# Kernel optimization log

Measured on AMD Instinct MI355X. Metric: run time of the kernel, lower is better.

Reference implementation:

```python
import jax, jax.numpy as jnp
import numpy as np

NUM_HEADS = 16
NUM_KV_HEADS = 4
HEAD_DIM = 128
BASE_THETA = 10000.0


def _rope_cos_sin(seq_len, head_dim, dtype):
    # standard (ntk_alpha=1) rotate-half RoPE tables: [S, head_dim]
    inv_freq = 1.0 / (BASE_THETA ** (jnp.arange(0, head_dim, 2, dtype=jnp.float32) / head_dim))
    angles = jnp.arange(seq_len, dtype=jnp.float32)[:, None] * inv_freq[None, :]  # [S, D/2]
    cos = jnp.concatenate([jnp.cos(angles), jnp.cos(angles)], axis=-1).astype(dtype)
    sin = jnp.concatenate([jnp.sin(angles), jnp.sin(angles)], axis=-1).astype(dtype)
    return cos, sin


def _rotate_half(t):
    half = t.shape[-1] // 2
    return jnp.concatenate([-t[..., half:], t[..., :half]], axis=-1)


def setup_inputs() -> dict:
    key = jax.random.key(0)
    ks = jax.random.split(key, 5)
    B, S, E = 2, 2048, 2048
    KV = NUM_KV_HEADS * HEAD_DIM  # 512
    scale = 0.02
    return {
        "x": jax.random.normal(ks[0], (B, S, E), dtype=jnp.float32),
        "Wq": jax.random.normal(ks[1], (E, E), dtype=jnp.float32) * scale,
        "Wk": jax.random.normal(ks[2], (E, KV), dtype=jnp.float32) * scale,
        "Wv": jax.random.normal(ks[3], (E, KV), dtype=jnp.float32) * scale,
        "Wo": jax.random.normal(ks[4], (E, E), dtype=jnp.float32) * scale,
    }


def reference(x, Wq, Wk, Wv, Wo):
    B, S, E = x.shape
    n_rep = NUM_HEADS // NUM_KV_HEADS
    scale = 1.0 / jnp.sqrt(jnp.float32(HEAD_DIM))

    # QKV projections (bias=False)
    q = (x @ Wq).reshape(B, S, NUM_HEADS, HEAD_DIM)
    k = (x @ Wk).reshape(B, S, NUM_KV_HEADS, HEAD_DIM)
    v = (x @ Wv).reshape(B, S, NUM_KV_HEADS, HEAD_DIM)

    # dynamic RoPE on q, k
    cos, sin = _rope_cos_sin(S, HEAD_DIM, x.dtype)
    cos = cos[None, :, None, :]
    sin = sin[None, :, None, :]
    q = q * cos + _rotate_half(q) * sin
    k = k * cos + _rotate_half(k) * sin

    # GQA: repeat kv heads to match query heads
    k = jnp.repeat(k, n_rep, axis=2)
    v = jnp.repeat(v, n_rep, axis=2)

    # [B, H, S, D]
    q = q.transpose(0, 2, 1, 3)
    k = k.transpose(0, 2, 1, 3)
    v = v.transpose(0, 2, 1, 3)

    # causal mask (window_size=0 -> standard causal, additive float mask)
    i = jnp.arange(S)[:, None]
    j = jnp.arange(S)[None, :]
    neg = jnp.finfo(jnp.float32).min
    causal = jnp.where(j > i, neg, 0.0).astype(jnp.float32)  # [S, S]

    scores = jnp.einsum("bhqd,bhkd->bhqk", q, k) * scale
    scores = scores + causal[None, None, :, :]
    weights = jax.nn.softmax(scores.astype(jnp.float32), axis=-1)
    attn = jnp.einsum("bhqk,bhkd->bhqd", weights.astype(v.dtype), v)

    attn = attn.transpose(0, 2, 1, 3).reshape(B, S, E)
    return attn @ Wo
```

## Files before the change

### kernel.cpp

```cpp
#include <hip/hip_runtime.h>
#include <math.h>


typedef __attribute__((ext_vector_type(8))) short short8;
typedef __attribute__((ext_vector_type(4))) float f32x4;

typedef const __attribute__((address_space(1))) void* gvp;
typedef __attribute__((address_space(3))) void* svp;

__device__ __forceinline__ void async16(const void* g, void* l) {
  __builtin_amdgcn_global_load_lds((gvp)g, (svp)l, 16, 0, 0);
}
__device__ __forceinline__ void wait_vm0() { asm volatile("s_waitcnt vmcnt(0)" ::: "memory"); }
__device__ __forceinline__ void barrier_raw() { asm volatile("s_barrier" ::: "memory"); }

__device__ __forceinline__ unsigned short f2b(float f) {
  unsigned int u = __builtin_bit_cast(unsigned int, f);
  u += 0x7fffu + ((u >> 16) & 1u);
  return (unsigned short)(u >> 16);
}
__device__ __forceinline__ float b2f(unsigned short h) {
  unsigned int u = ((unsigned int)h) << 16;
  return __builtin_bit_cast(float, u);
}

__global__ __launch_bounds__(256) void convx(const float* __restrict__ x,
                                             unsigned short* __restrict__ xb) {
  int i = blockIdx.x * 256 + threadIdx.x;
  const float4* p = (const float4*)x + (size_t)i * 2;
  float4 a = p[0], b4 = p[1];
  union { short8 v; unsigned short u[8]; } o;
  o.u[0] = f2b(a.x);  o.u[1] = f2b(a.y);  o.u[2] = f2b(a.z);  o.u[3] = f2b(a.w);
  o.u[4] = f2b(b4.x); o.u[5] = f2b(b4.y); o.u[6] = f2b(b4.z); o.u[7] = f2b(b4.w);
  ((short8*)xb)[i] = o.v;
}

__global__ __launch_bounds__(256) void wconv_all(const float* __restrict__ Wq,
                                                 const float* __restrict__ Wk,
                                                 const float* __restrict__ Wv,
                                                 const float* __restrict__ Wo,
                                                 unsigned short* __restrict__ WqkvT,
                                                 unsigned short* __restrict__ WoT) {
  __shared__ float t[32][33];
  int idx = blockIdx.x;
  const float* W; unsigned short* WT; int N, tx, ty;
  const int K = 2048;
  if (idx < 4096)      { W = Wq; WT = WqkvT;                         N = 2048; idx -= 0;    tx = idx & 63; ty = idx >> 6; }
  else if (idx < 5120) { W = Wk; WT = WqkvT + (size_t)2048 * 2048;   N = 512;  idx -= 4096; tx = idx & 15; ty = idx >> 4; }
  else if (idx < 6144) { W = Wv; WT = WqkvT + (size_t)2560 * 2048;   N = 512;  idx -= 5120; tx = idx & 15; ty = idx >> 4; }
  else                 { W = Wo; WT = WoT;                           N = 2048; idx -= 6144; tx = idx & 63; ty = idx >> 6; }
  int c = threadIdx.x & 31, r0 = threadIdx.x >> 5;
  int k0 = ty * 32, n0 = tx * 32;
#pragma unroll
  for (int r = r0; r < 32; r += 8) t[r][c] = W[(size_t)(k0 + r) * N + n0 + c];
  __syncthreads();
#pragma unroll
  for (int r = r0; r < 32; r += 8) WT[(size_t)(n0 + r) * K + k0 + c] = f2b(t[c][r]);
}

__global__ __launch_bounds__(256) void gemm_bt(const unsigned short* __restrict__ A,
                                               const unsigned short* __restrict__ BT,
                                               void* __restrict__ Cout,
                                               int M, int N, int K, int out_bf16) {
  const int n0 = blockIdx.x * 128;
  const int m0 = blockIdx.y * 128;
  const int tid = threadIdx.x;
  const int w = tid >> 6, lane = tid & 63, l15 = lane & 15, quad = lane >> 4;
  const int wm = w >> 1, wn = w & 1;

  __shared__ __align__(16) unsigned short As[2][128 * 64];
  __shared__ __align__(16) unsigned short Bs[2][128 * 64];

  f32x4 acc[4][4];
#pragma unroll
  for (int mi = 0; mi < 4; mi++)
#pragma unroll
    for (int ni = 0; ni < 4; ni++) acc[mi][ni] = (f32x4){0.f, 0.f, 0.f, 0.f};

  const int rl = lane >> 3;
  const int cl = lane & 7;
  const unsigned short* Ab = A + (size_t)m0 * K;
  const unsigned short* Bb = BT + (size_t)n0 * K;

#pragma unroll
  for (int i = 0; i < 4; i++) {
    int row = w * 32 + i * 8 + rl;
    int gc = cl ^ (row & 7);
    async16(Ab + (size_t)row * K + gc * 8, &As[0][(w * 32 + i * 8) * 64]);
    async16(Bb + (size_t)row * K + gc * 8, &Bs[0][(w * 32 + i * 8) * 64]);
  }

  const int nIter = K >> 6;
  for (int j = 0; j < nIter; j++) {
    wait_vm0();
    barrier_raw();
    const int cur = j & 1;

    if (j + 1 < nIter) {
      int kb = (j + 1) * 64;
#pragma unroll
      for (int i = 0; i < 4; i++) {
        int row = w * 32 + i * 8 + rl;
        int gc = cl ^ (row & 7);
        async16(Ab + (size_t)row * K + kb + gc * 8, &As[cur ^ 1][(w * 32 + i * 8) * 64]);
        async16(Bb + (size_t)row * K + kb + gc * 8, &Bs[cur ^ 1][(w * 32 + i * 8) * 64]);
      }
    }

    const unsigned short* as = &As[cur][0];
    const unsigned short* bs = &Bs[cur][0];
#pragma unroll
    for (int kk = 0; kk < 2; kk++) {
      short8 af[4], bfv[4];
#pragma unroll
      for (int mi = 0; mi < 4; mi++) {
        int row = wm * 64 + mi * 16 + l15;
        af[mi] = *(const short8*)&as[row * 64 + (((kk * 4 + quad) ^ (row & 7)) * 8)];
      }
#pragma unroll
      for (int ni = 0; ni < 4; ni++) {
        int row = wn * 64 + ni * 16 + l15;
        bfv[ni] = *(const short8*)&bs[row * 64 + (((kk * 4 + quad) ^ (row & 7)) * 8)];
      }
#pragma unroll
      for (int mi = 0; mi < 4; mi++)
#pragma unroll
        for (int ni = 0; ni < 4; ni++)
          acc[mi][ni] = __builtin_amdgcn_mfma_f32_16x16x32_bf16(af[mi], bfv[ni],
                                                                acc[mi][ni], 0, 0, 0);
    }
  }

  if (out_bf16) {
    unsigned short* C = (unsigned short*)Cout;
#pragma unroll
    for (int mi = 0; mi < 4; mi++)
#pragma unroll
      for (int ni = 0; ni < 4; ni++)
#pragma unroll
        for (int r = 0; r < 4; r++) {
          int row = m0 + wm * 64 + mi * 16 + quad * 4 + r;
          int col = n0 + wn * 64 + ni * 16 + l15;
          C[(size_t)row * N + col] = f2b(acc[mi][ni][r]);
        }
  } else {
    float* C = (float*)Cout;
#pragma unroll
    for (int mi = 0; mi < 4; mi++)
#pragma unroll
      for (int ni = 0; ni < 4; ni++)
#pragma unroll
        for (int r = 0; r < 4; r++) {
          int row = m0 + wm * 64 + mi * 16 + quad * 4 + r;
          int col = n0 + wn * 64 + ni * 16 + l15;
          C[(size_t)row * N + col] = acc[mi][ni][r];
        }
  }
}

#define SC_TOT 0.12753785056274918f
__global__ __launch_bounds__(256) void rope_kernel(const unsigned short* __restrict__ qkv,
                                                   unsigned short* __restrict__ Q,
                                                   unsigned short* __restrict__ Kd) {
  int b = blockIdx.z, hh = blockIdx.y;
  int tid = threadIdx.x;
  int d = tid & 63, sl = tid >> 6;
  int s = blockIdx.x * 4 + sl;
  const unsigned short* src = qkv + ((size_t)(b * 2048 + s)) * 3072 + hh * 128;
  float lo = b2f(src[d]), hi = b2f(src[d + 64]);
  float invf = exp2f(-0.20762050593046f * (float)d);
  float ang = (float)s * invf;
  float sn, cs;
  sincosf(ang, &sn, &cs);
  float nlo = lo * cs - hi * sn;
  float nhi = hi * cs + lo * sn;
  unsigned short* dst;
  if (hh < 16) {
    nlo *= SC_TOT; nhi *= SC_TOT;
    dst = Q + ((size_t)((b * 16 + hh) * 2048 + s)) * 128;
  } else {
    dst = Kd + ((size_t)((b * 4 + (hh - 16)) * 2048 + s)) * 128;
  }
  dst[d] = f2b(nlo);
  dst[d + 64] = f2b(nhi);
}

__global__ __launch_bounds__(256) void vtrans(const unsigned short* __restrict__ qkv,
                                              unsigned short* __restrict__ Vt) {
  int bkv = blockIdx.z;
  int b = bkv >> 2, kv = bkv & 3;
  int s0 = blockIdx.x * 64, d0 = blockIdx.y * 64;
  __shared__ unsigned short t[64][65];
  int c = threadIdx.x & 63, r0 = threadIdx.x >> 6;
  const unsigned short* src = qkv + ((size_t)(b * 2048 + s0)) * 3072 + 2560 + kv * 128 + d0;
#pragma unroll
  for (int r = r0; r < 64; r += 4) t[r][c] = src[(size_t)r * 3072 + c];
  __syncthreads();
  unsigned short* dst = Vt + ((size_t)bkv * 128 + d0) * 2048 + s0;
#pragma unroll
  for (int r = r0; r < 64; r += 4) dst[(size_t)r * 2048 + c] = t[c][r];
}

#define FIXED_M 12.0f
__global__ __launch_bounds__(256) void flash2(const unsigned short* __restrict__ Q,
                                              const unsigned short* __restrict__ Kc,
                                              const unsigned short* __restrict__ Vt,
                                              unsigned short* __restrict__ attn) {
  const int pair = blockIdx.x;
  const int h = blockIdx.y;
  const int b = blockIdx.z;
  const int kvh = h >> 2;
  const int tid = threadIdx.x;
  const int w = tid >> 6, lane = tid & 63, l15 = lane & 15, quad = lane >> 4;

  __shared__ __align__(16) unsigned short kbuf[2][64 * 128];
  __shared__ __align__(16) unsigned short vbuf[2][128 * 64];
  __shared__ __align__(16) unsigned short pbuf[4][16 * 64];

  const unsigned short* Qb = Q  + ((size_t)(b * 16 + h)) * 2048 * 128;
  const unsigned short* Kb = Kc + ((size_t)(b * 4 + kvh)) * 2048 * 128;
  const unsigned short* Vb = Vt + ((size_t)(b * 4 + kvh)) * 128 * 2048;
  unsigned short* pb = &pbuf[w][0];

  for (int t = 0; t < 2; t++) {
    const int qt = (t == 0) ? pair : (31 - pair);
    const int q0 = qt * 64;
    const int nT = qt + 1;

    short8 qf[4];
    {
      const unsigned short* qp = Qb + (size_t)(q0 + w * 16 + l15) * 128 + quad * 8;
#pragma unroll
      for (int kk = 0; kk < 4; kk++) qf[kk] = *(const short8*)(qp + kk * 32);
    }

    float l_i[4];
    f32x4 o[8];
#pragma unroll
    for (int r = 0; r < 4; r++) l_i[r] = 0.f;
#pragma unroll
    for (int nn = 0; nn < 8; nn++) o[nn] = (f32x4){0.f, 0.f, 0.f, 0.f};

    barrier_raw();

#pragma unroll
    for (int k = 0; k < 4; k++) {
      int m = w * 4 + k;
      int rl = m * 4 + (lane >> 4);
      int c8 = (lane & 15) ^ (rl & 7);
      async16(Kb + (size_t)rl * 128 + c8 * 8, &kbuf[0][m * 512]);
    }
#pragma unroll
    for (int k = 0; k < 4; k++) {
      int m = w * 4 + k;
      int d = m * 8 + (lane >> 3);
      int c3 = (lane & 7) ^ (d & 7);
      async16(Vb + (size_t)d * 2048 + c3 * 8, &vbuf[0][m * 512]);
    }

    for (int j = 0; j < nT; j++) {
      wait_vm0();
      barrier_raw();
      const int cur = j & 1;

      if (j + 1 < nT) {
        int j1 = (j + 1) * 64;
#pragma unroll
        for (int k = 0; k < 4; k++) {
          int m = w * 4 + k;
          int rl = m * 4 + (lane >> 4);
          int c8 = (lane & 15) ^ (rl & 7);
          async16(Kb + (size_t)(j1 + rl) * 128 + c8 * 8, &kbuf[cur ^ 1][m * 512]);
        }
#pragma unroll
        for (int k = 0; k < 4; k++) {
          int m = w * 4 + k;
          int d = m * 8 + (lane >> 3);
          int c3 = (lane & 7) ^ (d & 7);
          async16(Vb + (size_t)d * 2048 + (j + 1) * 64 + c3 * 8, &vbuf[cur ^ 1][m * 512]);
        }
      }

      const unsigned short* kb = &kbuf[cur][0];
      const unsigned short* vb = &vbuf[cur][0];

      f32x4 s4[4];
#pragma unroll
      for (int nn = 0; nn < 4; nn++) {
        f32x4 a = (f32x4){0.f, 0.f, 0.f, 0.f};
        int row = nn * 16 + l15;
#pragma unroll
        for (int kk = 0; kk < 4; kk++) {
          short8 bfr = *(const short8*)&kb[row * 128 + (((kk * 4 + quad) ^ (row & 7)) * 8)];
          a = __builtin_amdgcn_mfma_f32_16x16x32_bf16(qf[kk], bfr, a, 0, 0, 0);
        }
        s4[nn] = a;
      }

      const bool diag = (j * 64 == q0);
      const int myrow = w * 16 + quad * 4;
#pragma unroll
      for (int nn = 0; nn < 4; nn++) {
        int col = nn * 16 + l15;
#pragma unroll
        for (int r = 0; r < 4; r++) {
          float p = exp2f(s4[nn][r] - FIXED_M);
          if (diag && (col > myrow + r)) p = 0.f;
          l_i[r] += p;
          int prow = quad * 4 + r;
          pb[prow * 64 + ((nn * 2 + (l15 >> 3)) ^ (prow & 7)) * 8 + (l15 & 7)] = f2b(p);
        }
      }

#pragma unroll
      for (int ks = 0; ks < 2; ks++) {
        short8 af = *(const short8*)&pb[l15 * 64 + (((ks * 4 + quad) ^ (l15 & 7)) * 8)];
#pragma unroll
        for (int nn = 0; nn < 8; nn++) {
          int d = nn * 16 + l15;
          short8 bfr = *(const short8*)&vb[d * 64 + (((ks * 4 + quad) ^ (d & 7)) * 8)];
          o[nn] = __builtin_amdgcn_mfma_f32_16x16x32_bf16(af, bfr, o[nn], 0, 0, 0);
        }
      }
    }

#pragma unroll
    for (int r = 0; r < 4; r++) {
#pragma unroll
      for (int off = 1; off < 16; off <<= 1) l_i[r] += __shfl_xor(l_i[r], off, 64);
    }
    float inv[4];
#pragma unroll
    for (int r = 0; r < 4; r++) inv[r] = 1.f / l_i[r];
    unsigned short* ap = attn + ((size_t)(b * 2048 + q0 + w * 16)) * 2048 + h * 128;
#pragma unroll
    for (int nn = 0; nn < 8; nn++)
#pragma unroll
      for (int r = 0; r < 4; r++)
        ap[(size_t)(quad * 4 + r) * 2048 + nn * 16 + l15] = f2b(o[nn][r] * inv[r]);
  }
}

extern "C" void kernel_launch(void* const* d_in, const int* in_sizes, int n_in,
                              void* d_out, int out_size, void* d_ws, size_t ws_size,
                              hipStream_t stream) {
  const float* x  = (const float*)d_in[0];
  const float* Wq = (const float*)d_in[1];
  const float* Wk = (const float*)d_in[2];
  const float* Wv = (const float*)d_in[3];
  const float* Wo = (const float*)d_in[4];
  float* out = (float*)d_out;

  char* ws = (char*)d_ws;
  unsigned short* xb    = (unsigned short*)(ws);
  unsigned short* WqkvT = (unsigned short*)(ws + 16777216);
  unsigned short* WoT   = (unsigned short*)(ws + 29360128);
  unsigned short* qkv   = (unsigned short*)(ws + 37748736);
  unsigned short* Qm    = (unsigned short*)(ws + 62914560);
  unsigned short* Km    = (unsigned short*)(ws + 79691776);
  unsigned short* Vtm   = (unsigned short*)(ws + 83886080);
  unsigned short* attn  = xb;

  convx<<<4096, 256, 0, stream>>>(x, xb);
  wconv_all<<<10240, 256, 0, stream>>>(Wq, Wk, Wv, Wo, WqkvT, WoT);

  gemm_bt<<<dim3(24, 32), 256, 0, stream>>>(xb, WqkvT, qkv, 4096, 3072, 2048, 1);

  rope_kernel<<<dim3(512, 20, 2), 256, 0, stream>>>(qkv, Qm, Km);
  vtrans<<<dim3(32, 2, 8), 256, 0, stream>>>(qkv, Vtm);

  flash2<<<dim3(16, 16, 2), 256, 0, stream>>>(Qm, Km, Vtm, attn);

  gemm_bt<<<dim3(16, 32), 256, 0, stream>>>(attn, WoT, out, 4096, 2048, 2048, 0);
}
```

Baseline: 312.7 us.

## Rewrite flash attention with 32x32 MFMA and register-resident P via permlane swaps

```diff
diff --git a/kernel.cpp b/kernel.cpp
--- a/kernel.cpp
+++ b/kernel.cpp
@@ -4,6 +4,7 @@
 
 typedef __attribute__((ext_vector_type(8))) short short8;
 typedef __attribute__((ext_vector_type(4))) float f32x4;
+typedef __attribute__((ext_vector_type(16))) float f32x16;
 
 typedef const __attribute__((address_space(1))) void* gvp;
 typedef __attribute__((address_space(3))) void* svp;
@@ -22,6 +23,15 @@
 __device__ __forceinline__ float b2f(unsigned short h) {
   unsigned int u = ((unsigned int)h) << 16;
   return __builtin_bit_cast(float, u);
+}
+
+__device__ __forceinline__ unsigned int pk_bf16(float a, float b) {
+  unsigned int r;
+  asm("v_cvt_pk_bf16_f32 %0, %1, %2" : "=v"(r) : "v"(a), "v"(b));
+  return r;
+}
+__device__ __forceinline__ void plswap(unsigned int& a, unsigned int& b) {
+  asm("v_permlane32_swap_b32 %0, %1" : "+v"(a), "+v"(b));
 }
 
 __global__ __launch_bounds__(256) void convx(const float* __restrict__ x,
@@ -202,142 +212,157 @@
 }
 
 #define FIXED_M 12.0f
-__global__ __launch_bounds__(256) void flash2(const unsigned short* __restrict__ Q,
-                                              const unsigned short* __restrict__ Kc,
-                                              const unsigned short* __restrict__ Vt,
-                                              unsigned short* __restrict__ attn) {
-  const int pair = blockIdx.x;
+
+__device__ __forceinline__ void proc_acc(const f32x16& s, bool msk, int kvb, int q,
+                                         float& l_own, short8& paL, short8& paH) {
+  float p[16];
+#pragma unroll
+  for (int r = 0; r < 16; r++) {
+    float v = exp2f(s[r] - FIXED_M);
+    if (msk) {
+      int kv = kvb + (r & 3) + 8 * (r >> 2);
+      if (kv > q) v = 0.f;
+    }
+    p[r] = v;
+    l_own += v;
+  }
+  unsigned int u0 = pk_bf16(p[0], p[1]),  u1 = pk_bf16(p[2], p[3]);
+  unsigned int u2 = pk_bf16(p[4], p[5]),  u3 = pk_bf16(p[6], p[7]);
+  plswap(u0, u2); plswap(u1, u3);
+  unsigned int w0 = pk_bf16(p[8], p[9]),  w1 = pk_bf16(p[10], p[11]);
+  unsigned int w2 = pk_bf16(p[12], p[13]), w3 = pk_bf16(p[14], p[15]);
+  plswap(w0, w2); plswap(w1, w3);
+  union { unsigned int u[4]; short8 s8; } a, b;
+  a.u[0] = u0; a.u[1] = u1; a.u[2] = u2; a.u[3] = u3;
+  b.u[0] = w0; b.u[1] = w1; b.u[2] = w2; b.u[3] = w3;
+  paL = a.s8; paH = b.s8;
+}
+
+__global__ __launch_bounds__(256, 2) void flash2(const unsigned short* __restrict__ Q,
+                                                 const unsigned short* __restrict__ Kc,
+                                                 const unsigned short* __restrict__ Vt,
+                                                 unsigned short* __restrict__ attn) {
+  const int qt = 15 - blockIdx.x;
   const int h = blockIdx.y;
   const int b = blockIdx.z;
   const int kvh = h >> 2;
   const int tid = threadIdx.x;
-  const int w = tid >> 6, lane = tid & 63, l15 = lane & 15, quad = lane >> 4;
+  const int w = tid >> 6, lane = tid & 63;
+  const int l31 = lane & 31, hi = lane >> 5, x7 = l31 & 7;
 
   __shared__ __align__(16) unsigned short kbuf[2][64 * 128];
   __shared__ __align__(16) unsigned short vbuf[2][128 * 64];
-  __shared__ __align__(16) unsigned short pbuf[4][16 * 64];
+  __shared__ __align__(16) float li[4][32];
 
   const unsigned short* Qb = Q  + ((size_t)(b * 16 + h)) * 2048 * 128;
   const unsigned short* Kb = Kc + ((size_t)(b * 4 + kvh)) * 2048 * 128;
   const unsigned short* Vb = Vt + ((size_t)(b * 4 + kvh)) * 128 * 2048;
-  unsigned short* pb = &pbuf[w][0];
-
-  for (int t = 0; t < 2; t++) {
-    const int qt = (t == 0) ? pair : (31 - pair);
-    const int q0 = qt * 64;
-    const int nT = qt + 1;
-
-    short8 qf[4];
-    {
-      const unsigned short* qp = Qb + (size_t)(q0 + w * 16 + l15) * 128 + quad * 8;
-#pragma unroll
-      for (int kk = 0; kk < 4; kk++) qf[kk] = *(const short8*)(qp + kk * 32);
-    }
-
-    float l_i[4];
-    f32x4 o[8];
-#pragma unroll
-    for (int r = 0; r < 4; r++) l_i[r] = 0.f;
-#pragma unroll
-    for (int nn = 0; nn < 8; nn++) o[nn] = (f32x4){0.f, 0.f, 0.f, 0.f};
-
+
+  const int q0 = qt * 128;
+  const int qw = q0 + w * 32;
+  const int qv = qw + l31;
+  const int nT = 2 * qt + 2;
+
+  short8 qf[8];
+  {
+    const unsigned short* qp = Qb + (size_t)qv * 128 + hi * 8;
+#pragma unroll
+    for (int s = 0; s < 8; s++) qf[s] = *(const short8*)(qp + s * 16);
+  }
+
+  f32x16 o[4];
+#pragma unroll
+  for (int d = 0; d < 4; d++)
+#pragma unroll
+    for (int e = 0; e < 16; e++) o[d][e] = 0.f;
+  float l_own = 0.f;
+
+#pragma unroll
+  for (int k2 = 0; k2 < 4; k2++) {
+    int m = w * 4 + k2;
+    int rl = m * 4 + (lane >> 4);
+    int c8 = (lane & 15) ^ (rl & 7);
+    async16(Kb + (size_t)rl * 128 + c8 * 8, &kbuf[0][m * 512]);
+  }
+#pragma unroll
+  for (int k2 = 0; k2 < 4; k2++) {
+    int m = w * 4 + k2;
+    int d = m * 8 + (lane >> 3);
+    int c3 = (lane & 7) ^ (d & 7);
+    async16(Vb + (size_t)d * 2048 + c3 * 8, &vbuf[0][m * 512]);
+  }
+
+  for (int j = 0; j < nT; j++) {
+    wait_vm0();
     barrier_raw();
-
-#pragma unroll
-    for (int k = 0; k < 4; k++) {
-      int m = w * 4 + k;
-      int rl = m * 4 + (lane >> 4);
-      int c8 = (lane & 15) ^ (rl & 7);
-      async16(Kb + (size_t)rl * 128 + c8 * 8, &kbuf[0][m * 512]);
-    }
-#pragma unroll
-    for (int k = 0; k < 4; k++) {
-      int m = w * 4 + k;
-      int d = m * 8 + (lane >> 3);
-      int c3 = (lane & 7) ^ (d & 7);
-      async16(Vb + (size_t)d * 2048 + c3 * 8, &vbuf[0][m * 512]);
-    }
-
-    for (int j = 0; j < nT; j++) {
-      wait_vm0();
-      barrier_raw();
-      const int cur = j & 1;
-
-      if (j + 1 < nT) {
-        int j1 = (j + 1) * 64;
-#pragma unroll
-        for (int k = 0; k < 4; k++) {
-          int m = w * 4 + k;
-          int rl = m * 4 + (lane >> 4);
-          int c8 = (lane & 15) ^ (rl & 7);
-          async16(Kb + (size_t)(j1 + rl) * 128 + c8 * 8, &kbuf[cur ^ 1][m * 512]);
-        }
-#pragma unroll
-        for (int k = 0; k < 4; k++) {
-          int m = w * 4 + k;
-          int d = m * 8 + (lane >> 3);
-          int c3 = (lane & 7) ^ (d & 7);
-          async16(Vb + (size_t)d * 2048 + (j + 1) * 64 + c3 * 8, &vbuf[cur ^ 1][m * 512]);
-        }
-      }
-
-      const unsigned short* kb = &kbuf[cur][0];
-      const unsigned short* vb = &vbuf[cur][0];
-
-      f32x4 s4[4];
-#pragma unroll
-      for (int nn = 0; nn < 4; nn++) {
-        f32x4 a = (f32x4){0.f, 0.f, 0.f, 0.f};
-        int row = nn * 16 + l15;
-#pragma unroll
-        for (int kk = 0; kk < 4; kk++) {
-          short8 bfr = *(const short8*)&kb[row * 128 + (((kk * 4 + quad) ^ (row & 7)) * 8)];
-          a = __builtin_amdgcn_mfma_f32_16x16x32_bf16(qf[kk], bfr, a, 0, 0, 0);
-        }
-        s4[nn] = a;
-      }
-
-      const bool diag = (j * 64 == q0);
-      const int myrow = w * 16 + quad * 4;
-#pragma unroll
-      for (int nn = 0; nn < 4; nn++) {
-        int col = nn * 16 + l15;
-#pragma unroll
-        for (int r = 0; r < 4; r++) {
-          float p = exp2f(s4[nn][r] - FIXED_M);
-          if (diag && (col > myrow + r)) p = 0.f;
-          l_i[r] += p;
-          int prow = quad * 4 + r;
-          pb[prow * 64 + ((nn * 2 + (l15 >> 3)) ^ (prow & 7)) * 8 + (l15 & 7)] = f2b(p);
-        }
-      }
-
-#pragma unroll
-      for (int ks = 0; ks < 2; ks++) {
-        short8 af = *(const short8*)&pb[l15 * 64 + (((ks * 4 + quad) ^ (l15 & 7)) * 8)];
-#pragma unroll
-        for (int nn = 0; nn < 8; nn++) {
-          int d = nn * 16 + l15;
-          short8 bfr = *(const short8*)&vb[d * 64 + (((ks * 4 + quad) ^ (d & 7)) * 8)];
-          o[nn] = __builtin_amdgcn_mfma_f32_16x16x32_bf16(af, bfr, o[nn], 0, 0, 0);
-        }
-      }
-    }
-
-#pragma unroll
-    for (int r = 0; r < 4; r++) {
-#pragma unroll
-      for (int off = 1; off < 16; off <<= 1) l_i[r] += __shfl_xor(l_i[r], off, 64);
-    }
-    float inv[4];
-#pragma unroll
-    for (int r = 0; r < 4; r++) inv[r] = 1.f / l_i[r];
-    unsigned short* ap = attn + ((size_t)(b * 2048 + q0 + w * 16)) * 2048 + h * 128;
-#pragma unroll
-    for (int nn = 0; nn < 8; nn++)
-#pragma unroll
-      for (int r = 0; r < 4; r++)
-        ap[(size_t)(quad * 4 + r) * 2048 + nn * 16 + l15] = f2b(o[nn][r] * inv[r]);
+    const int cur = j & 1;
+    const int kb = j * 64;
+
+    if (j + 1 < nT) {
+      int kb2 = kb + 64;
+#pragma unroll
+      for (int k2 = 0; k2 < 4; k2++) {
+        int m = w * 4 + k2;
+        int rl = m * 4 + (lane >> 4);
+        int c8 = (lane & 15) ^ (rl & 7);
+        async16(Kb + (size_t)(kb2 + rl) * 128 + c8 * 8, &kbuf[cur ^ 1][m * 512]);
+      }
+#pragma unroll
+      for (int k2 = 0; k2 < 4; k2++) {
+        int m = w * 4 + k2;
+        int d = m * 8 + (lane >> 3);
+        int c3 = (lane & 7) ^ (d & 7);
+        async16(Vb + (size_t)d * 2048 + kb2 + c3 * 8, &vbuf[cur ^ 1][m * 512]);
+      }
+    }
+
+    if (kb > qw + 31) continue;
+
+    f32x16 sA, sB;
+#pragma unroll
+    for (int e = 0; e < 16; e++) { sA[e] = 0.f; sB[e] = 0.f; }
+    const unsigned short* kp = &kbuf[cur][0];
+#pragma unroll
+    for (int s = 0; s < 8; s++) {
+      int ch = (((s << 1) | hi) ^ x7) << 3;
+      short8 ka = *(const short8*)&kp[l31 * 128 + ch];
+      short8 kB = *(const short8*)&kp[(32 + l31) * 128 + ch];
+      sA = __builtin_amdgcn_mfma_f32_32x32x16_bf16(ka, qf[s], sA, 0, 0, 0);
+      sB = __builtin_amdgcn_mfma_f32_32x32x16_bf16(kB, qf[s], sB, 0, 0, 0);
+    }
+
+    const bool msk = (kb + 63 > qw);
+    short8 pa[4];
+    proc_acc(sA, msk, kb + 4 * hi, qv, l_own, pa[0], pa[1]);
+    proc_acc(sB, msk, kb + 32 + 4 * hi, qv, l_own, pa[2], pa[3]);
+
+    const unsigned short* vp = &vbuf[cur][0];
+#pragma unroll
+    for (int db = 0; db < 4; db++) {
+      int ro = (db * 32 + l31) * 64;
+#pragma unroll
+      for (int f = 0; f < 4; f++) {
+        int ch = (((f << 1) | hi) ^ x7) << 3;
+        short8 vf = *(const short8*)&vp[ro + ch];
+        o[db] = __builtin_amdgcn_mfma_f32_32x32x16_bf16(pa[f], vf, o[db], 0, 0, 0);
+      }
+    }
+  }
+
+  float l_tot = l_own + __shfl_xor(l_own, 32);
+  if (hi == 0) li[w][l31] = 1.f / l_tot;
+  f32x4 inv4[4];
+#pragma unroll
+  for (int t = 0; t < 4; t++) inv4[t] = *(const f32x4*)&li[w][t * 8 + 4 * hi];
+
+  unsigned short* ap0 = attn + ((size_t)(b * 2048 + qw)) * 2048 + h * 128 + l31;
+#pragma unroll
+  for (int db = 0; db < 4; db++) {
+#pragma unroll
+    for (int r = 0; r < 16; r++) {
+      int rowq = (r & 3) + 8 * (r >> 2) + 4 * hi;
+      ap0[(size_t)rowq * 2048 + db * 32] = f2b(o[db][r] * inv4[r >> 2][r & 3]);
+    }
   }
 }
 
```

After: 335.0 us. 7.1% more time.
